# Kernel optimization log

Measured on AMD Instinct MI355X. Metric: run time of the kernel, lower is better.

## Reference

```python
import jax, jax.numpy as jnp
import numpy as np

# AQLM-style additive multi-codebook quantization of an 8192x8192 weight
O_GROUPS, I_GROUPS, N_CB = 8192, 1024, 2
CB_SIZE, OG, IG = 65536, 1, 8  # 16-bit codebooks, out_group_size=1, in_group_size=8


def setup_inputs() -> dict:
    key = jax.random.key(0)
    k1, k2, k3 = jax.random.split(key, 3)
    codes = jax.random.randint(k1, (O_GROUPS, I_GROUPS, N_CB), 0, CB_SIZE, dtype=jnp.int32)
    codebooks = jax.random.normal(k2, (N_CB, CB_SIZE, OG, IG), dtype=jnp.float32)
    scales = jax.random.uniform(k3, (O_GROUPS, 1, 1, 1), dtype=jnp.float32)
    return {"codes": codes, "codebooks": codebooks, "scales": scales}


def reference(codes, codebooks, scales):
    # codes: [O, I, n_cb] int32; codebooks: [n_cb, K, og, ig]; scales: [O, 1, 1, 1]
    n_cb, cb_size, og, ig = codebooks.shape
    o_groups, i_groups, _ = codes.shape
    # per-codebook gather (F.embedding_bag sum == gather each codebook then sum)
    gathered = jax.vmap(lambda cb, c: cb[c], in_axes=(0, 2))(codebooks, codes)  # [n_cb, O, I, og, ig]
    recon = gathered.sum(axis=0) * scales                                       # [O, I, og, ig]
    # swapaxes(-3, -2) then flatten groups -> [out_features, in_features]
    return recon.swapaxes(1, 2).reshape(o_groups * og, i_groups * ig)
```

## Files before the change

### kernel.cpp

```cpp
#include <hip/hip_runtime.h>


#define O_GROUPS 8192
#define I_GROUPS 1024
#define CB_SIZE  65536
#define BATCH    4

typedef float f32x4 __attribute__((ext_vector_type(4)));
typedef int   i32x2 __attribute__((ext_vector_type(2)));

__global__ __launch_bounds__(256) void aqlm_dequant_kernel(
    const i32x2* __restrict__ codes,
    const f32x4* __restrict__ cb,
    const float* __restrict__ scales,
    f32x4*       __restrict__ out)
{
    const int tid  = threadIdx.x;
    const int base = blockIdx.x * (256 * BATCH) + tid;

    int   slot[BATCH];
    i32x2 c[BATCH];
    #pragma unroll
    for (int k = 0; k < BATCH; ++k) {
        slot[k] = base + k * 256;
        c[k] = __builtin_nontemporal_load(&codes[slot[k] >> 1]);
    }

    f32x4 a[BATCH], b[BATCH];
    #pragma unroll
    for (int k = 0; k < BATCH; ++k) {
        const int h = slot[k] & 1;
        a[k] = cb[(size_t)c[k].x * 2 + h];
        b[k] = cb[((size_t)CB_SIZE + c[k].y) * 2 + h];
    }

    #pragma unroll
    for (int k = 0; k < BATCH; ++k) {
        const float s = scales[slot[k] >> 11];
        f32x4 r = (a[k] + b[k]) * s;
        __builtin_nontemporal_store(r, &out[slot[k]]);
    }
}

extern "C" void kernel_launch(void* const* d_in, const int* in_sizes, int n_in,
                              void* d_out, int out_size, void* d_ws, size_t ws_size,
                              hipStream_t stream) {
    const i32x2* codes  = (const i32x2*)d_in[0];
    const f32x4* cb     = (const f32x4*)d_in[1];
    const float* scales = (const float*)d_in[2];
    f32x4*       out    = (f32x4*)d_out;

    const int total_slots = O_GROUPS * I_GROUPS * 2;
    const int block = 256;
    const int grid  = total_slots / (block * BATCH);
    aqlm_dequant_kernel<<<grid, block, 0, stream>>>(codes, cb, scales, out);
}
```

Measured before the change: 127.6 us.

## Convert codebooks to bf16 in workspace and gather one 16-byte entry per group

Result: slower. 131.4 us (+3.0%).

```diff
diff --git a/kernel.cpp b/kernel.cpp
--- a/kernel.cpp
+++ b/kernel.cpp
@@ -6,10 +6,72 @@
 #define CB_SIZE  65536
 #define BATCH    4
 
-typedef float f32x4 __attribute__((ext_vector_type(4)));
-typedef int   i32x2 __attribute__((ext_vector_type(2)));
+typedef float          f32x4 __attribute__((ext_vector_type(4)));
+typedef int            i32x2 __attribute__((ext_vector_type(2)));
+typedef unsigned short u16x4 __attribute__((ext_vector_type(4)));
+typedef unsigned short u16x8 __attribute__((ext_vector_type(8)));
 
-__global__ __launch_bounds__(256) void aqlm_dequant_kernel(
+__device__ __forceinline__ unsigned short f2bf(float f) {
+    unsigned int u = __float_as_uint(f);
+    u += 0x7FFF + ((u >> 16) & 1);
+    return (unsigned short)(u >> 16);
+}
+__device__ __forceinline__ float bf2f(unsigned short h) {
+    return __uint_as_float((unsigned int)h << 16);
+}
+
+__global__ __launch_bounds__(256) void cb_convert_kernel(
+    const f32x4* __restrict__ cb, u16x4* __restrict__ cbh)
+{
+    const int i = blockIdx.x * 256 + threadIdx.x;
+    f32x4 v = cb[i];
+    u16x4 h;
+    h.x = f2bf(v.x); h.y = f2bf(v.y); h.z = f2bf(v.z); h.w = f2bf(v.w);
+    cbh[i] = h;
+}
+
+__global__ __launch_bounds__(256) void aqlm_dequant_bf16_kernel(
+    const i32x2* __restrict__ codes,
+    const u16x8* __restrict__ cbh,
+    const float* __restrict__ scales,
+    f32x4*       __restrict__ out)
+{
+    const int tid  = threadIdx.x;
+    const int base = blockIdx.x * (256 * BATCH) + tid;
+
+    int   g[BATCH];
+    i32x2 c[BATCH];
+    #pragma unroll
+    for (int k = 0; k < BATCH; ++k) {
+        g[k] = base + k * 256;
+        c[k] = __builtin_nontemporal_load(&codes[g[k]]);
+    }
+
+    u16x8 a[BATCH], b[BATCH];
+    #pragma unroll
+    for (int k = 0; k < BATCH; ++k) {
+        a[k] = cbh[c[k].x];
+        b[k] = cbh[CB_SIZE + c[k].y];
+    }
+
+    #pragma unroll
+    for (int k = 0; k < BATCH; ++k) {
+        const float s = scales[g[k] >> 10];
+        f32x4 r0, r1;
+        r0.x = (bf2f(a[k][0]) + bf2f(b[k][0])) * s;
+        r0.y = (bf2f(a[k][1]) + bf2f(b[k][1])) * s;
+        r0.z = (bf2f(a[k][2]) + bf2f(b[k][2])) * s;
+        r0.w = (bf2f(a[k][3]) + bf2f(b[k][3])) * s;
+        r1.x = (bf2f(a[k][4]) + bf2f(b[k][4])) * s;
+        r1.y = (bf2f(a[k][5]) + bf2f(b[k][5])) * s;
+        r1.z = (bf2f(a[k][6]) + bf2f(b[k][6])) * s;
+        r1.w = (bf2f(a[k][7]) + bf2f(b[k][7])) * s;
+        __builtin_nontemporal_store(r0, &out[(size_t)g[k] * 2]);
+        __builtin_nontemporal_store(r1, &out[(size_t)g[k] * 2 + 1]);
+    }
+}
+
+__global__ __launch_bounds__(256) void aqlm_dequant_f32_kernel(
     const i32x2* __restrict__ codes,
     const f32x4* __restrict__ cb,
     const float* __restrict__ scales,
@@ -17,7 +79,6 @@
 {
     const int tid  = threadIdx.x;
     const int base = blockIdx.x * (256 * BATCH) + tid;
-
     int   slot[BATCH];
     i32x2 c[BATCH];
     #pragma unroll
@@ -25,7 +86,6 @@
         slot[k] = base + k * 256;
         c[k] = __builtin_nontemporal_load(&codes[slot[k] >> 1]);
     }
-
     f32x4 a[BATCH], b[BATCH];
     #pragma unroll
     for (int k = 0; k < BATCH; ++k) {
@@ -33,7 +93,6 @@
         a[k] = cb[(size_t)c[k].x * 2 + h];
         b[k] = cb[((size_t)CB_SIZE + c[k].y) * 2 + h];
     }
-
     #pragma unroll
     for (int k = 0; k < BATCH; ++k) {
         const float s = scales[slot[k] >> 11];
@@ -46,12 +105,21 @@
                               void* d_out, int out_size, void* d_ws, size_t ws_size,
                               hipStream_t stream) {
     const i32x2* codes  = (const i32x2*)d_in[0];
-    const f32x4* cb     = (const f32x4*)d_in[1];
     const float* scales = (const float*)d_in[2];
     f32x4*       out    = (f32x4*)d_out;
 
-    const int total_slots = O_GROUPS * I_GROUPS * 2;
-    const int block = 256;
-    const int grid  = total_slots / (block * BATCH);
-    aqlm_dequant_kernel<<<grid, block, 0, stream>>>(codes, cb, scales, out);
+    const size_t cbh_bytes = (size_t)2 * CB_SIZE * 8 * 2;
+    if (ws_size >= cbh_bytes) {
+        cb_convert_kernel<<<1024, 256, 0, stream>>>((const f32x4*)d_in[1],
+                                                    (u16x4*)d_ws);
+        const int total_groups = O_GROUPS * I_GROUPS;
+        const int grid = total_groups / (256 * BATCH);
+        aqlm_dequant_bf16_kernel<<<grid, 256, 0, stream>>>(
+            codes, (const u16x8*)d_ws, scales, out);
+    } else {
+        const int total_slots = O_GROUPS * I_GROUPS * 2;
+        const int grid = total_slots / (256 * BATCH);
+        aqlm_dequant_f32_kernel<<<grid, 256, 0, stream>>>(
+            codes, (const f32x4*)d_in[1], scales, out);
+    }
 }
```
